# Kernel tuning notes

Measured on AMD Instinct MI355X. Metric: run time of the kernel, lower is better.

## Reference

```python
import jax, jax.numpy as jnp
import numpy as np

N_HEADS = 12
HEAD_DIM = 64
HIDDEN = 768


def _split_heads(t):
    # [B, S, H*D] -> [B, H, S, D]
    b, s, _ = t.shape
    return t.reshape(b, s, N_HEADS, HEAD_DIM).transpose(0, 2, 1, 3)


def setup_inputs() -> dict:
    key = jax.random.key(0)
    B, S = 4, 2048
    x = jax.random.normal(key, (B, S, 3 * HIDDEN), dtype=jnp.float32)
    # GPT-2 causal bias buffer: lower-triangular True = attend
    causal_mask = jnp.tril(jnp.ones((S, S), dtype=bool))[None, None, :, :]
    return {"input": x, "causal_mask": causal_mask}


def reference(input, causal_mask):
    query, key, value = jnp.split(input, 3, axis=2)  # each [B, S, 768]
    q = _split_heads(query)   # [B, H, S, D]
    k = _split_heads(key)
    v = _split_heads(value)
    scale = jnp.asarray(HEAD_DIM ** 0.5, dtype=q.dtype)
    attn_weights = jnp.einsum('bhqd,bhkd->bhqk', q, k) / scale
    mask_value = jnp.finfo(attn_weights.dtype).min
    attn_weights = jnp.where(causal_mask, attn_weights, mask_value)
    attn_weights = jax.nn.softmax(attn_weights, axis=-1).astype(v.dtype)
    # attn_dropout(p=0.1) is identity in eval mode; omitted for determinism
    attn_output = jnp.einsum('bhqk,bhkd->bhqd', attn_weights, v)
    return (attn_output, attn_weights)
```

## Files before the change

kernel.cpp:

```cpp
#include <hip/hip_runtime.h>
#include <hip/hip_bf16.h>


#define S_LEN 2048
#define DH    64
#define NHD   12
#define H3    2304
#define QT    64
#define KTILE 64
#define NT    32
#define PSTR  72
#define OSZ   (4 * NHD * S_LEN * DH)

typedef __attribute__((ext_vector_type(8))) short short8;
typedef __attribute__((ext_vector_type(4))) float f32x4;

__device__ __forceinline__ short bfc(float x) {
  return (short)__builtin_bit_cast(unsigned short, __float2bfloat16(x));
}
__device__ __forceinline__ float b2f(unsigned short u) {
  return __builtin_bit_cast(float, (unsigned int)u << 16);
}
__device__ __forceinline__ short8 cvt8(const float* p) {
  const float4 a = *(const float4*)p;
  const float4 b = *(const float4*)(p + 4);
  short8 r;
  r[0] = bfc(a.x); r[1] = bfc(a.y); r[2] = bfc(a.z); r[3] = bfc(a.w);
  r[4] = bfc(b.x); r[5] = bfc(b.y); r[6] = bfc(b.z); r[7] = bfc(b.w);
  return r;
}

__global__ __launch_bounds__(256)
void attn_fused(const void* __restrict__ xv, void* __restrict__ ov)
{
  __shared__ __align__(16) unsigned short k_lds[KTILE * DH];
  __shared__ __align__(16) unsigned short v_lds[KTILE * DH];
  __shared__ __align__(16) unsigned short p_lds[QT * PSTR];

  const int tid  = threadIdx.x;
  const int wave = tid >> 6;
  const int lane = tid & 63;
  const int quad = lane >> 4;
  const int l16  = lane & 15;

  const unsigned int* xw = (const unsigned int*)xv;
  int cnt = 0;
  #pragma unroll
  for (int j = 0; j < 32; ++j) {
    const unsigned e = (xw[j] >> 7) & 0xFFu;
    cnt += (e >= 100u && e <= 150u) ? 1 : 0;
  }
  const bool isf32 = (cnt < 24);

  const unsigned short* xh = (const unsigned short*)xv;
  const float*          xf = (const float*)xv;

  const int qb = (NT - 1) - blockIdx.x;
  const int bh = blockIdx.y;
  const int b  = bh / NHD;
  const int h  = bh - b * NHD;
  const int q_base = qb * QT;

  const int qrow = q_base + wave * 16 + l16;
  const size_t qoff = (size_t)(b * S_LEN + qrow) * H3 + h * DH + quad * 8;
  short8 qa0, qa1;
  if (isf32) { qa0 = cvt8(xf + qoff); qa1 = cvt8(xf + qoff + 32); }
  else       { qa0 = *(const short8*)(xh + qoff);
               qa1 = *(const short8*)(xh + qoff + 32); }

  const int c0 = tid,     c1 = tid + 256;
  const int r0 = c0 >> 3, o0 = (c0 & 7) * 8;
  const int r1 = c1 >> 3, o1 = (c1 & 7) * 8;
  const size_t koff0 = ((size_t)b * S_LEN + r0) * H3 + 768 + h * DH + o0;
  const size_t koff1 = ((size_t)b * S_LEN + r1) * H3 + 768 + h * DH + o1;

  const int qg0 = q_base + wave * 16 + quad * 4;

  auto compute_scores = [&](int kt, float (&sc)[4][4]) {
    #pragma unroll
    for (int n16 = 0; n16 < 4; ++n16) {
      const unsigned short* kr = &k_lds[(n16 * 16 + l16) * DH + quad * 8];
      const short8 kb0 = *(const short8*)kr;
      const short8 kb1 = *(const short8*)(kr + 32);
      f32x4 acc = {0.f, 0.f, 0.f, 0.f};
      acc = __builtin_amdgcn_mfma_f32_16x16x32_bf16(qa0, kb0, acc, 0, 0, 0);
      acc = __builtin_amdgcn_mfma_f32_16x16x32_bf16(qa1, kb1, acc, 0, 0, 0);
      const int keyg = kt * KTILE + n16 * 16 + l16;
      #pragma unroll
      for (int r = 0; r < 4; ++r)
        sc[n16][r] = (keyg <= qg0 + r) ? acc[r] * 0.125f : -1e30f;
    }
  };

  float m_r[4], l_r[4];
  #pragma unroll
  for (int r = 0; r < 4; ++r) { m_r[r] = -1e30f; l_r[r] = 0.f; }

  for (int kt = 0; kt <= qb; ++kt) {
    __syncthreads();
    const size_t t = (size_t)kt * KTILE * H3;
    short8 s0, s1;
    if (isf32) { s0 = cvt8(xf + koff0 + t); s1 = cvt8(xf + koff1 + t); }
    else       { s0 = *(const short8*)(xh + koff0 + t);
                 s1 = *(const short8*)(xh + koff1 + t); }
    *(short8*)&k_lds[c0 * 8] = s0;
    *(short8*)&k_lds[c1 * 8] = s1;
    __syncthreads();

    float sc[4][4];
    compute_scores(kt, sc);

    #pragma unroll
    for (int r = 0; r < 4; ++r) {
      float tmax = fmaxf(fmaxf(sc[0][r], sc[1][r]), fmaxf(sc[2][r], sc[3][r]));
      #pragma unroll
      for (int sh = 1; sh < 16; sh <<= 1)
        tmax = fmaxf(tmax, __shfl_xor(tmax, sh, 64));
      const float mn = fmaxf(m_r[r], tmax);
      float ps = __expf(sc[0][r] - mn) + __expf(sc[1][r] - mn)
               + __expf(sc[2][r] - mn) + __expf(sc[3][r] - mn);
      #pragma unroll
      for (int sh = 1; sh < 16; sh <<= 1)
        ps += __shfl_xor(ps, sh, 64);
      l_r[r] = l_r[r] * __expf(m_r[r] - mn) + ps;
      m_r[r] = mn;
    }
  }

  float invl[4];
  #pragma unroll
  for (int r = 0; r < 4; ++r) invl[r] = 1.f / l_r[r];

  f32x4 o_acc[4];
  #pragma unroll
  for (int m16 = 0; m16 < 4; ++m16) o_acc[m16] = (f32x4){0.f, 0.f, 0.f, 0.f};

  const size_t wbase = ((size_t)bh * S_LEN + q_base + wave * 16) * S_LEN;
  float*          wrF = (float*)ov + OSZ + wbase;
  unsigned short* wrH = (unsigned short*)ov + OSZ + wbase;

  for (int kt = 0; kt <= qb; ++kt) {
    __syncthreads();
    const size_t t = (size_t)kt * KTILE * H3;
    short8 s0, s1, u0, u1;
    if (isf32) {
      s0 = cvt8(xf + koff0 + t);       s1 = cvt8(xf + koff1 + t);
      u0 = cvt8(xf + koff0 + t + 768); u1 = cvt8(xf + koff1 + t + 768);
    } else {
      s0 = *(const short8*)(xh + koff0 + t);
      s1 = *(const short8*)(xh + koff1 + t);
      u0 = *(const short8*)(xh + koff0 + t + 768);
      u1 = *(const short8*)(xh + koff1 + t + 768);
    }
    *(short8*)&k_lds[c0 * 8] = s0;  *(short8*)&k_lds[c1 * 8] = s1;
    *(short8*)&v_lds[c0 * 8] = u0;  *(short8*)&v_lds[c1 * 8] = u1;
    __syncthreads();

    float sc[4][4];
    compute_scores(kt, sc);

    #pragma unroll
    for (int n16 = 0; n16 < 4; ++n16) {
      #pragma unroll
      for (int r = 0; r < 4; ++r) {
        const float p = __expf(sc[n16][r] - m_r[r]) * invl[r];
        p_lds[(wave * 16 + quad * 4 + r) * PSTR + n16 * 16 + l16] =
            (unsigned short)bfc(p);
      }
    }
    __syncthreads();

    const unsigned short* pr = &p_lds[(wave * 16 + l16) * PSTR + quad * 8];
    const short8 pb0 = *(const short8*)pr;
    const short8 pb1 = *(const short8*)(pr + 32);

    #pragma unroll
    for (int m16 = 0; m16 < 4; ++m16) {
      short8 va0, va1;
      #pragma unroll
      for (int j = 0; j < 8; ++j) {
        va0[j] = (short)v_lds[(quad * 8 + j) * DH + m16 * 16 + l16];
        va1[j] = (short)v_lds[(quad * 8 + j + 32) * DH + m16 * 16 + l16];
      }
      o_acc[m16] = __builtin_amdgcn_mfma_f32_16x16x32_bf16(va0, pb0, o_acc[m16], 0, 0, 0);
      o_acc[m16] = __builtin_amdgcn_mfma_f32_16x16x32_bf16(va1, pb1, o_acc[m16], 0, 0, 0);
    }

    #pragma unroll
    for (int i = 0; i < 2; ++i) {
      const int c = lane + i * 64;
      const int row = c >> 3, col8 = c & 7;
      const short8 pw = *(const short8*)&p_lds[(wave * 16 + row) * PSTR + col8 * 8];
      if (isf32) {
        float* d = wrF + (size_t)row * S_LEN + kt * KTILE + col8 * 8;
        *(float4*)d       = make_float4(b2f(pw[0]), b2f(pw[1]), b2f(pw[2]), b2f(pw[3]));
        *(float4*)(d + 4) = make_float4(b2f(pw[4]), b2f(pw[5]), b2f(pw[6]), b2f(pw[7]));
      } else {
        *(short8*)&wrH[(size_t)row * S_LEN + kt * KTILE + col8 * 8] = pw;
      }
    }
  }

  for (int kt = qb + 1; kt < NT; ++kt) {
    #pragma unroll
    for (int i = 0; i < 2; ++i) {
      const int c = lane + i * 64;
      const int row = c >> 3, col8 = c & 7;
      if (isf32) {
        float* d = wrF + (size_t)row * S_LEN + kt * KTILE + col8 * 8;
        *(float4*)d       = make_float4(0.f, 0.f, 0.f, 0.f);
        *(float4*)(d + 4) = make_float4(0.f, 0.f, 0.f, 0.f);
      } else {
        const short8 zz = {0, 0, 0, 0, 0, 0, 0, 0};
        *(short8*)&wrH[(size_t)row * S_LEN + kt * KTILE + col8 * 8] = zz;
      }
    }
  }

  const size_t obase = ((size_t)bh * S_LEN + q_base + wave * 16 + l16) * DH;
  #pragma unroll
  for (int m16 = 0; m16 < 4; ++m16) {
    #pragma unroll
    for (int r = 0; r < 4; ++r) {
      const int d = m16 * 16 + quad * 4 + r;
      if (isf32) ((float*)ov)[obase + d] = o_acc[m16][r];
      else ((unsigned short*)ov)[obase + d] = (unsigned short)bfc(o_acc[m16][r]);
    }
  }
}

extern "C" void kernel_launch(void* const* d_in, const int* in_sizes, int n_in,
                              void* d_out, int out_size, void* d_ws, size_t ws_size,
                              hipStream_t stream) {
  dim3 grid(NT, 4 * NHD);
  attn_fused<<<grid, 256, 0, stream>>>(d_in[0], d_out);
}
```

Before: 1.157 ms.

## Prefetch K/V tiles into registers, swizzle LDS, transpose V, templatize dtype, nontemporal stores

Register-prefetches the next K/V tile while the current tile is processed, and adds XOR swizzles to the K and V LDS layouts. V is stored transposed, so the PV operands come from vector LDS reads instead of scalar gathers. The kernel is templated on dtype and launched twice, with the non-matching variant exiting early; one __syncthreads is replaced by an lgkmcnt wait. All global stores become nontemporal, and the output is written as vectors. The trade-offs are an extra launch, more registers, and a weakened barrier that only works if each wave reads only the P rows it wrote itself.

New measurement: 1.066 ms. -7.9%, faster.

```diff
diff --git a/kernel.cpp b/kernel.cpp
--- a/kernel.cpp
+++ b/kernel.cpp
@@ -10,9 +10,11 @@
 #define KTILE 64
 #define NT    32
 #define PSTR  72
+#define VSTR  72
 #define OSZ   (4 * NHD * S_LEN * DH)
 
 typedef __attribute__((ext_vector_type(8))) short short8;
+typedef __attribute__((ext_vector_type(4))) short short4e;
 typedef __attribute__((ext_vector_type(4))) float f32x4;
 
 __device__ __forceinline__ short bfc(float x) {
@@ -21,20 +23,19 @@
 __device__ __forceinline__ float b2f(unsigned short u) {
   return __builtin_bit_cast(float, (unsigned int)u << 16);
 }
-__device__ __forceinline__ short8 cvt8(const float* p) {
-  const float4 a = *(const float4*)p;
-  const float4 b = *(const float4*)(p + 4);
+__device__ __forceinline__ short8 pack8(const float4 a, const float4 b) {
   short8 r;
   r[0] = bfc(a.x); r[1] = bfc(a.y); r[2] = bfc(a.z); r[3] = bfc(a.w);
   r[4] = bfc(b.x); r[5] = bfc(b.y); r[6] = bfc(b.z); r[7] = bfc(b.w);
   return r;
 }
 
+template <int F32>
 __global__ __launch_bounds__(256)
 void attn_fused(const void* __restrict__ xv, void* __restrict__ ov)
 {
   __shared__ __align__(16) unsigned short k_lds[KTILE * DH];
-  __shared__ __align__(16) unsigned short v_lds[KTILE * DH];
+  __shared__ __align__(16) unsigned short v_lds[DH * VSTR];
   __shared__ __align__(16) unsigned short p_lds[QT * PSTR];
 
   const int tid  = threadIdx.x;
@@ -51,6 +52,7 @@
     cnt += (e >= 100u && e <= 150u) ? 1 : 0;
   }
   const bool isf32 = (cnt < 24);
+  if (isf32 != (bool)F32) return;
 
   const unsigned short* xh = (const unsigned short*)xv;
   const float*          xf = (const float*)xv;
@@ -64,24 +66,77 @@
   const int qrow = q_base + wave * 16 + l16;
   const size_t qoff = (size_t)(b * S_LEN + qrow) * H3 + h * DH + quad * 8;
   short8 qa0, qa1;
-  if (isf32) { qa0 = cvt8(xf + qoff); qa1 = cvt8(xf + qoff + 32); }
-  else       { qa0 = *(const short8*)(xh + qoff);
-               qa1 = *(const short8*)(xh + qoff + 32); }
-
-  const int c0 = tid,     c1 = tid + 256;
-  const int r0 = c0 >> 3, o0 = (c0 & 7) * 8;
-  const int r1 = c1 >> 3, o1 = (c1 & 7) * 8;
-  const size_t koff0 = ((size_t)b * S_LEN + r0) * H3 + 768 + h * DH + o0;
-  const size_t koff1 = ((size_t)b * S_LEN + r1) * H3 + 768 + h * DH + o1;
+  if constexpr (F32) {
+    qa0 = pack8(*(const float4*)(xf + qoff),      *(const float4*)(xf + qoff + 4));
+    qa1 = pack8(*(const float4*)(xf + qoff + 32), *(const float4*)(xf + qoff + 36));
+  } else {
+    qa0 = *(const short8*)(xh + qoff);
+    qa1 = *(const short8*)(xh + qoff + 32);
+  }
+
+  const int sl   = tid & 7;
+  const int row0 = tid >> 3;
+  const int ksl  = (sl ^ (row0 & 7)) << 3;
+  const int kwo0 = row0 * DH + ksl;
+  const int kwo1 = (row0 + 32) * DH + ksl;
+  const int vk0  = row0 ^ (sl << 3);
+  const int vk1  = (row0 + 32) ^ (sl << 3);
+  const size_t koff0 = ((size_t)b * S_LEN + row0) * H3 + 768 + h * DH + sl * 8;
+  const size_t koff1 = ((size_t)b * S_LEN + row0 + 32) * H3 + 768 + h * DH + sl * 8;
 
   const int qg0 = q_base + wave * 16 + quad * 4;
 
+  float4 fK[4]; short8 hK[2];
+  float4 fV[4]; short8 hV[2];
+
+  auto issueK = [&](int kt) {
+    const size_t t = (size_t)kt * KTILE * H3;
+    if constexpr (F32) {
+      fK[0] = *(const float4*)(xf + koff0 + t);
+      fK[1] = *(const float4*)(xf + koff0 + t + 4);
+      fK[2] = *(const float4*)(xf + koff1 + t);
+      fK[3] = *(const float4*)(xf + koff1 + t + 4);
+    } else {
+      hK[0] = *(const short8*)(xh + koff0 + t);
+      hK[1] = *(const short8*)(xh + koff1 + t);
+    }
+  };
+  auto issueV = [&](int kt) {
+    const size_t t = (size_t)kt * KTILE * H3 + 768;
+    if constexpr (F32) {
+      fV[0] = *(const float4*)(xf + koff0 + t);
+      fV[1] = *(const float4*)(xf + koff0 + t + 4);
+      fV[2] = *(const float4*)(xf + koff1 + t);
+      fV[3] = *(const float4*)(xf + koff1 + t + 4);
+    } else {
+      hV[0] = *(const short8*)(xh + koff0 + t);
+      hV[1] = *(const short8*)(xh + koff1 + t);
+    }
+  };
+  auto writeK = [&]() {
+    short8 s0, s1;
+    if constexpr (F32) { s0 = pack8(fK[0], fK[1]); s1 = pack8(fK[2], fK[3]); }
+    else               { s0 = hK[0];               s1 = hK[1]; }
+    *(short8*)&k_lds[kwo0] = s0;
+    *(short8*)&k_lds[kwo1] = s1;
+  };
+  auto writeV = [&]() {
+    short8 v0, v1;
+    if constexpr (F32) { v0 = pack8(fV[0], fV[1]); v1 = pack8(fV[2], fV[3]); }
+    else               { v0 = hV[0];               v1 = hV[1]; }
+    #pragma unroll
+    for (int j = 0; j < 8; ++j) {
+      v_lds[(sl * 8 + j) * VSTR + vk0] = (unsigned short)v0[j];
+      v_lds[(sl * 8 + j) * VSTR + vk1] = (unsigned short)v1[j];
+    }
+  };
+
   auto compute_scores = [&](int kt, float (&sc)[4][4]) {
     #pragma unroll
     for (int n16 = 0; n16 < 4; ++n16) {
-      const unsigned short* kr = &k_lds[(n16 * 16 + l16) * DH + quad * 8];
-      const short8 kb0 = *(const short8*)kr;
-      const short8 kb1 = *(const short8*)(kr + 32);
+      const unsigned short* krow = &k_lds[(n16 * 16 + l16) * DH];
+      const short8 kb0 = *(const short8*)(krow + (((quad    ) ^ (l16 & 7)) << 3));
+      const short8 kb1 = *(const short8*)(krow + (((quad + 4) ^ (l16 & 7)) << 3));
       f32x4 acc = {0.f, 0.f, 0.f, 0.f};
       acc = __builtin_amdgcn_mfma_f32_16x16x32_bf16(qa0, kb0, acc, 0, 0, 0);
       acc = __builtin_amdgcn_mfma_f32_16x16x32_bf16(qa1, kb1, acc, 0, 0, 0);
@@ -96,15 +151,11 @@
   #pragma unroll
   for (int r = 0; r < 4; ++r) { m_r[r] = -1e30f; l_r[r] = 0.f; }
 
+  issueK(0);
   for (int kt = 0; kt <= qb; ++kt) {
     __syncthreads();
-    const size_t t = (size_t)kt * KTILE * H3;
-    short8 s0, s1;
-    if (isf32) { s0 = cvt8(xf + koff0 + t); s1 = cvt8(xf + koff1 + t); }
-    else       { s0 = *(const short8*)(xh + koff0 + t);
-                 s1 = *(const short8*)(xh + koff1 + t); }
-    *(short8*)&k_lds[c0 * 8] = s0;
-    *(short8*)&k_lds[c1 * 8] = s1;
+    writeK();
+    if (kt < qb) issueK(kt + 1);
     __syncthreads();
 
     float sc[4][4];
@@ -139,21 +190,11 @@
   float*          wrF = (float*)ov + OSZ + wbase;
   unsigned short* wrH = (unsigned short*)ov + OSZ + wbase;
 
+  issueK(0); issueV(0);
   for (int kt = 0; kt <= qb; ++kt) {
     __syncthreads();
-    const size_t t = (size_t)kt * KTILE * H3;
-    short8 s0, s1, u0, u1;
-    if (isf32) {
-      s0 = cvt8(xf + koff0 + t);       s1 = cvt8(xf + koff1 + t);
-      u0 = cvt8(xf + koff0 + t + 768); u1 = cvt8(xf + koff1 + t + 768);
-    } else {
-      s0 = *(const short8*)(xh + koff0 + t);
-      s1 = *(const short8*)(xh + koff1 + t);
-      u0 = *(const short8*)(xh + koff0 + t + 768);
-      u1 = *(const short8*)(xh + koff1 + t + 768);
-    }
-    *(short8*)&k_lds[c0 * 8] = s0;  *(short8*)&k_lds[c1 * 8] = s1;
-    *(short8*)&v_lds[c0 * 8] = u0;  *(short8*)&v_lds[c1 * 8] = u1;
+    writeK(); writeV();
+    if (kt < qb) { issueK(kt + 1); issueV(kt + 1); }
     __syncthreads();
 
     float sc[4][4];
@@ -168,7 +209,7 @@
             (unsigned short)bfc(p);
       }
     }
-    __syncthreads();
+    asm volatile("s_waitcnt lgkmcnt(0)" ::: "memory");
 
     const unsigned short* pr = &p_lds[(wave * 16 + l16) * PSTR + quad * 8];
     const short8 pb0 = *(const short8*)pr;
@@ -176,12 +217,10 @@
 
     #pragma unroll
     for (int m16 = 0; m16 < 4; ++m16) {
-      short8 va0, va1;
-      #pragma unroll
-      for (int j = 0; j < 8; ++j) {
-        va0[j] = (short)v_lds[(quad * 8 + j) * DH + m16 * 16 + l16];
-        va1[j] = (short)v_lds[(quad * 8 + j + 32) * DH + m16 * 16 + l16];
-      }
+      const int sd = ((m16 << 1) + (l16 >> 3)) & 7;
+      const unsigned short* vrow = &v_lds[(m16 * 16 + l16) * VSTR];
+      const short8 va0 = *(const short8*)(vrow + ((quad ^ sd) << 3));
+      const short8 va1 = *(const short8*)(vrow + (((quad + 4) ^ sd) << 3));
       o_acc[m16] = __builtin_amdgcn_mfma_f32_16x16x32_bf16(va0, pb0, o_acc[m16], 0, 0, 0);
       o_acc[m16] = __builtin_amdgcn_mfma_f32_16x16x32_bf16(va1, pb1, o_acc[m16], 0, 0, 0);
     }
@@ -191,28 +230,33 @@
       const int c = lane + i * 64;
       const int row = c >> 3, col8 = c & 7;
       const short8 pw = *(const short8*)&p_lds[(wave * 16 + row) * PSTR + col8 * 8];
-      if (isf32) {
+      if (F32) {
         float* d = wrF + (size_t)row * S_LEN + kt * KTILE + col8 * 8;
-        *(float4*)d       = make_float4(b2f(pw[0]), b2f(pw[1]), b2f(pw[2]), b2f(pw[3]));
-        *(float4*)(d + 4) = make_float4(b2f(pw[4]), b2f(pw[5]), b2f(pw[6]), b2f(pw[7]));
+        f32x4 w0 = {b2f(pw[0]), b2f(pw[1]), b2f(pw[2]), b2f(pw[3])};
+        f32x4 w1 = {b2f(pw[4]), b2f(pw[5]), b2f(pw[6]), b2f(pw[7])};
+        __builtin_nontemporal_store(w0, (f32x4*)d);
+        __builtin_nontemporal_store(w1, (f32x4*)(d + 4));
       } else {
-        *(short8*)&wrH[(size_t)row * S_LEN + kt * KTILE + col8 * 8] = pw;
+        __builtin_nontemporal_store(
+            pw, (short8*)&wrH[(size_t)row * S_LEN + kt * KTILE + col8 * 8]);
       }
     }
   }
 
+  const f32x4 z4 = {0.f, 0.f, 0.f, 0.f};
+  const short8 z8 = {0, 0, 0, 0, 0, 0, 0, 0};
   for (int kt = qb + 1; kt < NT; ++kt) {
     #pragma unroll
     for (int i = 0; i < 2; ++i) {
       const int c = lane + i * 64;
       const int row = c >> 3, col8 = c & 7;
-      if (isf32) {
+      if (F32) {
         float* d = wrF + (size_t)row * S_LEN + kt * KTILE + col8 * 8;
-        *(float4*)d       = make_float4(0.f, 0.f, 0.f, 0.f);
-        *(float4*)(d + 4) = make_float4(0.f, 0.f, 0.f, 0.f);
+        __builtin_nontemporal_store(z4, (f32x4*)d);
+        __builtin_nontemporal_store(z4, (f32x4*)(d + 4));
       } else {
-        const short8 zz = {0, 0, 0, 0, 0, 0, 0, 0};
-        *(short8*)&wrH[(size_t)row * S_LEN + kt * KTILE + col8 * 8] = zz;
+        __builtin_nontemporal_store(
+            z8, (short8*)&wrH[(size_t)row * S_LEN + kt * KTILE + col8 * 8]);
       }
     }
   }
@@ -220,11 +264,14 @@
   const size_t obase = ((size_t)bh * S_LEN + q_base + wave * 16 + l16) * DH;
   #pragma unroll
   for (int m16 = 0; m16 < 4; ++m16) {
-    #pragma unroll
-    for (int r = 0; r < 4; ++r) {
-      const int d = m16 * 16 + quad * 4 + r;
-      if (isf32) ((float*)ov)[obase + d] = o_acc[m16][r];
-      else ((unsigned short*)ov)[obase + d] = (unsigned short)bfc(o_acc[m16][r]);
+    const int d = m16 * 16 + quad * 4;
+    if (F32) {
+      __builtin_nontemporal_store(o_acc[m16], (f32x4*)&((float*)ov)[obase + d]);
+    } else {
+      short4e o;
+      #pragma unroll
+      for (int r = 0; r < 4; ++r) o[r] = bfc(o_acc[m16][r]);
+      __builtin_nontemporal_store(o, (short4e*)&((unsigned short*)ov)[obase + d]);
     }
   }
 }
@@ -233,5 +280,6 @@
                               void* d_out, int out_size, void* d_ws, size_t ws_size,
                               hipStream_t stream) {
   dim3 grid(NT, 4 * NHD);
-  attn_fused<<<grid, 256, 0, stream>>>(d_in[0], d_out);
-}
+  attn_fused<1><<<grid, 256, 0, stream>>>(d_in[0], d_out);
+  attn_fused<0><<<grid, 256, 0, stream>>>(d_in[0], d_out);
+}
```
